# Kernel optimization log

Hardware: AMD Instinct MI355X
Metric: run time of the kernel (lower is better)

Reference implementation:

```python
import jax, jax.numpy as jnp
import numpy as np

QMAX = 7.0            # int4 narrow range: [-7, 7]
SCALING_MIN_VAL = 2e-16


def fake_quant_weight_per_channel(w):
    """Brevitas CommonIntWeightPerChannelQuant, bit_width=4.

    Per-output-channel float scale from abs-max stats, narrow-range signed
    int4 round+clamp, then dequantize. STE so gradients pass through.
    w: [O, I, KH, KW]
    """
    amax = jnp.max(jnp.abs(w), axis=(1, 2, 3), keepdims=True)   # [O,1,1,1]
    scale = jnp.maximum(amax / QMAX, SCALING_MIN_VAL)
    wq = jnp.clip(jnp.round(w / scale), -QMAX, QMAX) * scale
    # straight-through estimator (matches Brevitas round_ste backward)
    return w + jax.lax.stop_gradient(wq - w)


def setup_inputs() -> dict:
    key = jax.random.key(0)
    kx, kw = jax.random.split(key)
    x = jax.random.normal(kx, (32, 256, 56, 56), dtype=jnp.float32)
    # conv weight [out_channels, in_channels, kh, kw]
    w = jax.random.normal(kw, (256, 256, 3, 3), dtype=jnp.float32) * 0.05
    return {"x": x, "w": w}


def reference(x, w):
    wq = fake_quant_weight_per_channel(w)
    return jax.lax.conv_general_dilated(
        x, wq,
        window_strides=(1, 1),
        padding=((1, 1), (1, 1)),
        dimension_numbers=("NCHW", "OIHW", "NCHW"),
    )
```

## Files before the change

kernel.cpp:

```cpp
#include <hip/hip_runtime.h>
#include <cstdint>
#include <cstddef>

typedef __bf16 bf16x8 __attribute__((ext_vector_type(8)));
typedef float  f32x4  __attribute__((ext_vector_type(4)));
typedef int    i32x4  __attribute__((ext_vector_type(4)));

#define QMAX 7.0f
#define SCALE_MIN 2e-16f

__global__ __launch_bounds__(256) void quant_w_kernel(const float* __restrict__ w,
                                                      __bf16* __restrict__ wq) {
    const int o = blockIdx.x;
    const int t = threadIdx.x;
    const float* wo = w + (size_t)o * 2304;

    float vals[9];
    float m = 0.f;
    #pragma unroll
    for (int i = 0; i < 9; ++i) {
        float v = wo[t + i * 256];
        vals[i] = v;
        m = fmaxf(m, fabsf(v));
    }
    #pragma unroll
    for (int off = 32; off >= 1; off >>= 1) m = fmaxf(m, __shfl_down(m, off));
    __shared__ float red[4];
    __shared__ float s_scale;
    if ((t & 63) == 0) red[t >> 6] = m;
    __syncthreads();
    if (t == 0) {
        float am = fmaxf(fmaxf(red[0], red[1]), fmaxf(red[2], red[3]));
        s_scale = fmaxf(am / QMAX, SCALE_MIN);
    }
    __syncthreads();
    const float scale = s_scale;

    #pragma unroll
    for (int i = 0; i < 9; ++i) {
        int idx = t + i * 256;
        int c = idx / 9;
        int tap = idx - c * 9;
        float q = rintf(vals[i] / scale);
        q = fminf(QMAX, fmaxf(-QMAX, q));
        wq[(size_t)tap * 65536 + (size_t)o * 256 + c] = (__bf16)(q * scale);
    }
}

__global__ __launch_bounds__(256) void convert_x_kernel(const float* __restrict__ x,
                                                        __bf16* __restrict__ xpad) {
    __shared__ float tile[32][33];
    const int n  = blockIdx.z;
    const int c0 = blockIdx.y * 32;
    const int p0 = blockIdx.x * 32;
    const int tx = threadIdx.x & 31;
    const int ty = threadIdx.x >> 5;

    #pragma unroll
    for (int r = 0; r < 4; ++r) {
        int c = c0 + ty + r * 8;
        tile[ty + r * 8][tx] = x[((size_t)(n * 256 + c)) * 3136 + p0 + tx];
    }
    __syncthreads();
    #pragma unroll
    for (int r = 0; r < 4; ++r) {
        int p = p0 + ty + r * 8;
        int h = p / 56, wcol = p - h * 56;
        xpad[(((size_t)n * 58 + h + 1) * 58 + (wcol + 1)) * 256 + c0 + tx] =
            (__bf16)tile[tx][ty + r * 8];
    }
}

__global__ __launch_bounds__(256) void zero_halo_kernel(__bf16* __restrict__ xpad) {
    const int t = blockIdx.x * 256 + threadIdx.x;
    const int cvec = t & 31;
    const int r    = t >> 5;
    const int n    = r / 228;
    const int pos  = r - n * 228;
    if (n >= 32) return;
    int h, wcol;
    if      (pos < 58)  { h = 0;          wcol = pos; }
    else if (pos < 116) { h = 57;         wcol = pos - 58; }
    else if (pos < 172) { h = pos - 115;  wcol = 0; }
    else                { h = pos - 171;  wcol = 57; }
    i32x4* dst = (i32x4*)(xpad + (((size_t)n * 58 + h) * 58 + wcol) * 256);
    dst[cvec] = (i32x4){0, 0, 0, 0};
}

__device__ __forceinline__ void gload_lds16(const void* g, void* l) {
    __builtin_amdgcn_global_load_lds((const __attribute__((address_space(1))) void*)g,
                                     (__attribute__((address_space(3))) void*)l,
                                     16, 0, 0);
}

__global__ __launch_bounds__(256) void conv_mfma_kernel(const __bf16* __restrict__ xpad,
                                                        const __bf16* __restrict__ wq,
                                                        float* __restrict__ out) {
    __shared__ __align__(16) char Ash[128 * 128];
    __shared__ __align__(16) char Bsh[128 * 128];

    const int tid  = threadIdx.x;
    const int wv   = tid >> 6;
    const int lane = tid & 63;
    const int bp   = blockIdx.x;
    const int n    = bp / 25;
    const int p0   = (bp - n * 25) * 128;
    const int o0   = blockIdx.y * 128;

    const int srow   = wv * 8 + (lane >> 3);
    const int schunk = (lane & 7) ^ (lane >> 3);
    const int selem  = schunk * 8;

    const __bf16* pA = wq + (size_t)(o0 + srow) * 256 + selem;
    const __bf16* pB[4];
    #pragma unroll
    for (int j = 0; j < 4; ++j) {
        int p = p0 + srow + j * 32;
        if (p > 3135) p = 3135;
        int h = p / 56, wcol = p - h * 56;
        pB[j] = xpad + (((size_t)n * 58 + h) * 58 + wcol) * 256 + selem;
    }

    const int wr = wv >> 1;
    const int wc = wv & 1;

    const int a_rowbyte = (wr * 64 + (lane & 15)) * 128;
    const int b_rowbyte = (wc * 64 + (lane & 15)) * 128;
    int kx[2];
    #pragma unroll
    for (int s = 0; s < 2; ++s)
        kx[s] = ((s * 4 + (lane >> 4)) ^ (lane & 7)) * 16;

    f32x4 acc[4][4];
    #pragma unroll
    for (int m = 0; m < 4; ++m)
        #pragma unroll
        for (int nf = 0; nf < 4; ++nf)
            acc[m][nf] = (f32x4){0.f, 0.f, 0.f, 0.f};

    for (int tap = 0; tap < 9; ++tap) {
        const int kh = tap / 3, kw = tap - kh * 3;
        const size_t aoff0 = (size_t)tap * 65536;
        const size_t boff0 = (size_t)(kh * 58 + kw) * 256;
        #pragma unroll
        for (int cc = 0; cc < 4; ++cc) {
            const size_t aoff = aoff0 + cc * 64;
            const size_t boff = boff0 + cc * 64;
            #pragma unroll
            for (int j = 0; j < 4; ++j) {
                gload_lds16(pB[j] + boff, Bsh + (wv * 8 + j * 32) * 128);
                gload_lds16(pA + j * 8192 + aoff, Ash + (wv * 8 + j * 32) * 128);
            }
            __syncthreads();

            #pragma unroll
            for (int s = 0; s < 2; ++s) {
                bf16x8 a[4], b[4];
                #pragma unroll
                for (int m = 0; m < 4; ++m)
                    a[m] = *(const bf16x8*)(Ash + a_rowbyte + m * 2048 + kx[s]);
                #pragma unroll
                for (int nf = 0; nf < 4; ++nf)
                    b[nf] = *(const bf16x8*)(Bsh + b_rowbyte + nf * 2048 + kx[s]);
                #pragma unroll
                for (int m = 0; m < 4; ++m)
                    #pragma unroll
                    for (int nf = 0; nf < 4; ++nf)
                        acc[m][nf] = __builtin_amdgcn_mfma_f32_16x16x32_bf16(
                            a[m], b[nf], acc[m][nf], 0, 0, 0);
            }
            __syncthreads();
        }
    }

    #pragma unroll
    for (int m = 0; m < 4; ++m) {
        const int obase = o0 + wr * 64 + m * 16 + (lane >> 4) * 4;
        #pragma unroll
        for (int nf = 0; nf < 4; ++nf) {
            const int p = p0 + wc * 64 + nf * 16 + (lane & 15);
            if (p < 3136) {
                #pragma unroll
                for (int r = 0; r < 4; ++r)
                    out[((size_t)(n * 256 + obase + r)) * 3136 + p] = acc[m][nf][r];
            }
        }
    }
}

__global__ __launch_bounds__(256) void conv_naive_kernel(const float* __restrict__ x,
                                                         const float* __restrict__ w,
                                                         float* __restrict__ out) {
    const int n = blockIdx.z;
    const int o = blockIdx.y;
    const int strip = blockIdx.x;
    __shared__ float wqs[2304];
    __shared__ float red[4];
    __shared__ float s_scale;
    const float* wo = w + (size_t)o * 2304;
    float m = 0.f;
    for (int i = threadIdx.x; i < 2304; i += 256) m = fmaxf(m, fabsf(wo[i]));
    #pragma unroll
    for (int off = 32; off >= 1; off >>= 1) m = fmaxf(m, __shfl_down(m, off));
    if ((threadIdx.x & 63) == 0) red[threadIdx.x >> 6] = m;
    __syncthreads();
    if (threadIdx.x == 0) {
        float am = fmaxf(fmaxf(red[0], red[1]), fmaxf(red[2], red[3]));
        s_scale = fmaxf(am / QMAX, SCALE_MIN);
    }
    __syncthreads();
    const float scale = s_scale;
    for (int i = threadIdx.x; i < 2304; i += 256) {
        float q = rintf(wo[i] / scale);
        q = fminf(QMAX, fmaxf(-QMAX, q));
        wqs[i] = q * scale;
    }
    __syncthreads();
    int p = strip * 256 + threadIdx.x;
    if (p >= 3136) return;
    int h = p / 56, wcol = p - h * 56;
    float acc = 0.f;
    for (int c = 0; c < 256; ++c) {
        const float* xc = x + ((size_t)(n * 256 + c)) * 3136;
        const float* wk = wqs + c * 9;
        #pragma unroll
        for (int kh = 0; kh < 3; ++kh) {
            int hh = h + kh - 1;
            if (hh < 0 || hh > 55) continue;
            #pragma unroll
            for (int kw = 0; kw < 3; ++kw) {
                int ww2 = wcol + kw - 1;
                if (ww2 < 0 || ww2 > 55) continue;
                acc += xc[hh * 56 + ww2] * wk[kh * 3 + kw];
            }
        }
    }
    out[((size_t)(n * 256 + o)) * 3136 + p] = acc;
}

extern "C" void kernel_launch(void* const* d_in, const int* in_sizes, int n_in,
                              void* d_out, int out_size, void* d_ws, size_t ws_size,
                              hipStream_t stream) {
    const float* x = (const float*)d_in[0];
    const float* w = (const float*)d_in[1];
    float* out = (float*)d_out;

    const size_t WQ_BYTES   = 9ull * 256 * 256 * 2;
    const size_t XPAD_OFF   = WQ_BYTES;
    const size_t XPAD_BYTES = 32ull * 58 * 58 * 256 * 2;

    if (ws_size >= XPAD_OFF + XPAD_BYTES) {
        __bf16* wq   = (__bf16*)d_ws;
        __bf16* xpad = (__bf16*)((char*)d_ws + XPAD_OFF);
        zero_halo_kernel<<<912, 256, 0, stream>>>(xpad);
        quant_w_kernel<<<256, 256, 0, stream>>>(w, wq);
        convert_x_kernel<<<dim3(98, 8, 32), 256, 0, stream>>>(x, xpad);
        conv_mfma_kernel<<<dim3(800, 2), 256, 0, stream>>>(xpad, wq, out);
    } else {
        conv_naive_kernel<<<dim3(13, 256, 32), 256, 0, stream>>>(x, w, out);
    }
}
```

Measured before the change: 191.8 us.

## Rewrite conv GEMM as 256x256 double-buffered tile with 32x32 MFMA

```diff
diff --git a/kernel.cpp b/kernel.cpp
--- a/kernel.cpp
+++ b/kernel.cpp
@@ -4,10 +4,14 @@
 
 typedef __bf16 bf16x8 __attribute__((ext_vector_type(8)));
 typedef float  f32x4  __attribute__((ext_vector_type(4)));
+typedef float  f32x16 __attribute__((ext_vector_type(16)));
 typedef int    i32x4  __attribute__((ext_vector_type(4)));
 
 #define QMAX 7.0f
 #define SCALE_MIN 2e-16f
+
+#define BAR()    asm volatile("s_barrier" ::: "memory")
+#define WAITV0() asm volatile("s_waitcnt vmcnt(0)" ::: "memory")
 
 __global__ __launch_bounds__(256) void quant_w_kernel(const float* __restrict__ w,
                                                       __bf16* __restrict__ wq) {
@@ -93,96 +97,165 @@
                                      16, 0, 0);
 }
 
-__global__ __launch_bounds__(256) void conv_mfma_kernel(const __bf16* __restrict__ xpad,
-                                                        const __bf16* __restrict__ wq,
-                                                        float* __restrict__ out) {
-    __shared__ __align__(16) char Ash[128 * 128];
-    __shared__ __align__(16) char Bsh[128 * 128];
-
+__global__ __launch_bounds__(512, 2) void conv_mfma_kernel(const __bf16* __restrict__ xpad,
+                                                           const __bf16* __restrict__ wq,
+                                                           float* __restrict__ out) {
+    extern __shared__ __align__(16) char lds[];
     const int tid  = threadIdx.x;
     const int wv   = tid >> 6;
     const int lane = tid & 63;
-    const int bp   = blockIdx.x;
-    const int n    = bp / 25;
-    const int p0   = (bp - n * 25) * 128;
-    const int o0   = blockIdx.y * 128;
-
-    const int srow   = wv * 8 + (lane >> 3);
+    const int bid  = blockIdx.x;
+    const int swz  = (bid & 7) * 49 + (bid >> 3);
+    const int p0   = swz * 256;
+
+    const int wr = wv >> 2;
+    const int wc = wv & 3;
+
+    const int srow  = wv * 8 + (lane >> 3);
     const int schunk = (lane & 7) ^ (lane >> 3);
-    const int selem  = schunk * 8;
-
-    const __bf16* pA = wq + (size_t)(o0 + srow) * 256 + selem;
+    const __bf16* pAg = wq + (size_t)srow * 256 + schunk * 8;
     const __bf16* pB[4];
     #pragma unroll
-    for (int j = 0; j < 4; ++j) {
-        int p = p0 + srow + j * 32;
-        if (p > 3135) p = 3135;
-        int h = p / 56, wcol = p - h * 56;
-        pB[j] = xpad + (((size_t)n * 58 + h) * 58 + wcol) * 256 + selem;
-    }
-
-    const int wr = wv >> 1;
-    const int wc = wv & 1;
-
-    const int a_rowbyte = (wr * 64 + (lane & 15)) * 128;
-    const int b_rowbyte = (wc * 64 + (lane & 15)) * 128;
-    int kx[2];
-    #pragma unroll
-    for (int s = 0; s < 2; ++s)
-        kx[s] = ((s * 4 + (lane >> 4)) ^ (lane & 7)) * 16;
-
-    f32x4 acc[4][4];
+    for (int p = 0; p < 4; ++p) {
+        int pos = p0 + p * 64 + srow;
+        int ni = pos / 3136;
+        int hw = pos - ni * 3136;
+        int h = hw / 56, w = hw - h * 56;
+        pB[p] = xpad + (((size_t)ni * 58 + h) * 58 + w) * 256 + schunk * 8;
+    }
+
+    const int hi = lane >> 5;
+    int kxo[4];
+    #pragma unroll
+    for (int ks = 0; ks < 4; ++ks)
+        kxo[ks] = ((ks * 2 + hi) ^ (lane & 7)) * 16;
+    const int arowb = (wr * 128 + (lane & 31)) * 128;
+    const int browb = (wc * 64  + (lane & 31)) * 128;
+
+    f32x16 acc[4][2];
     #pragma unroll
     for (int m = 0; m < 4; ++m)
         #pragma unroll
-        for (int nf = 0; nf < 4; ++nf)
-            acc[m][nf] = (f32x4){0.f, 0.f, 0.f, 0.f};
-
-    for (int tap = 0; tap < 9; ++tap) {
-        const int kh = tap / 3, kw = tap - kh * 3;
-        const size_t aoff0 = (size_t)tap * 65536;
-        const size_t boff0 = (size_t)(kh * 58 + kw) * 256;
-        #pragma unroll
-        for (int cc = 0; cc < 4; ++cc) {
-            const size_t aoff = aoff0 + cc * 64;
-            const size_t boff = boff0 + cc * 64;
+        for (int n = 0; n < 2; ++n)
+            acc[m][n] = (f32x16)(0.f);
+
+    {
+        char* wa = lds;
+        char* wb = lds + 32768;
+        #pragma unroll
+        for (int p = 0; p < 4; ++p) {
+            gload_lds16(pAg + p * 16384, wa + (p * 64 + wv * 8) * 128);
+            gload_lds16(pB[p],           wb + (p * 64 + wv * 8) * 128);
+        }
+        WAITV0();
+        BAR();
+    }
+
+    for (int s = 0; s < 36; ++s) {
+        const int cur = s & 1;
+        const char* Ard = lds + (cur ? 65536 : 0);
+        const char* Brd = Ard + 32768;
+        char* Awr = lds + (cur ? 0 : 65536);
+        char* Bwr = Awr + 32768;
+        const bool stg = (s < 35);
+        int aoffN = 0, boffN = 0;
+        if (stg) {
+            const int sn = s + 1;
+            const int tapN = sn >> 2, ccN = sn & 3;
+            const int khN = tapN / 3, kwN = tapN - khN * 3;
+            aoffN = tapN * 65536 + ccN * 64;
+            boffN = (khN * 58 + kwN) * 256 + ccN * 64;
+        }
+
+        bf16x8 a0[4], a1[4], b0[4], b1[4];
+
+        if (stg) {
+            gload_lds16(pAg + 0 * 16384 + aoffN, Awr + (0 * 64 + wv * 8) * 128);
+            gload_lds16(pB[0] + boffN,           Bwr + (0 * 64 + wv * 8) * 128);
+        }
+        #pragma unroll
+        for (int ks = 0; ks < 4; ++ks) {
+            a0[ks] = *(const bf16x8*)(Ard + arowb + 0 * 4096 + kxo[ks]);
+            a1[ks] = *(const bf16x8*)(Ard + arowb + 1 * 4096 + kxo[ks]);
+            b0[ks] = *(const bf16x8*)(Brd + browb + 0 * 4096 + kxo[ks]);
+        }
+        BAR();
+        __builtin_amdgcn_s_setprio(1);
+        #pragma unroll
+        for (int ks = 0; ks < 4; ++ks) {
+            acc[0][0] = __builtin_amdgcn_mfma_f32_32x32x16_bf16(a0[ks], b0[ks], acc[0][0], 0, 0, 0);
+            acc[1][0] = __builtin_amdgcn_mfma_f32_32x32x16_bf16(a1[ks], b0[ks], acc[1][0], 0, 0, 0);
+        }
+        __builtin_amdgcn_s_setprio(0);
+        BAR();
+
+        if (stg) {
+            gload_lds16(pAg + 1 * 16384 + aoffN, Awr + (1 * 64 + wv * 8) * 128);
+            gload_lds16(pB[1] + boffN,           Bwr + (1 * 64 + wv * 8) * 128);
+        }
+        #pragma unroll
+        for (int ks = 0; ks < 4; ++ks)
+            b1[ks] = *(const bf16x8*)(Brd + browb + 1 * 4096 + kxo[ks]);
+        BAR();
+        __builtin_amdgcn_s_setprio(1);
+        #pragma unroll
+        for (int ks = 0; ks < 4; ++ks) {
+            acc[0][1] = __builtin_amdgcn_mfma_f32_32x32x16_bf16(a0[ks], b1[ks], acc[0][1], 0, 0, 0);
+            acc[1][1] = __builtin_amdgcn_mfma_f32_32x32x16_bf16(a1[ks], b1[ks], acc[1][1], 0, 0, 0);
+        }
+        __builtin_amdgcn_s_setprio(0);
+        BAR();
+
+        if (stg) {
+            gload_lds16(pAg + 2 * 16384 + aoffN, Awr + (2 * 64 + wv * 8) * 128);
+            gload_lds16(pB[2] + boffN,           Bwr + (2 * 64 + wv * 8) * 128);
+        }
+        #pragma unroll
+        for (int ks = 0; ks < 4; ++ks) {
+            a0[ks] = *(const bf16x8*)(Ard + arowb + 2 * 4096 + kxo[ks]);
+            a1[ks] = *(const bf16x8*)(Ard + arowb + 3 * 4096 + kxo[ks]);
+        }
+        BAR();
+        __builtin_amdgcn_s_setprio(1);
+        #pragma unroll
+        for (int ks = 0; ks < 4; ++ks) {
+            acc[2][0] = __builtin_amdgcn_mfma_f32_32x32x16_bf16(a0[ks], b0[ks], acc[2][0], 0, 0, 0);
+            acc[3][0] = __builtin_amdgcn_mfma_f32_32x32x16_bf16(a1[ks], b0[ks], acc[3][0], 0, 0, 0);
+        }
+        __builtin_amdgcn_s_setprio(0);
+        BAR();
+
+        if (stg) {
+            gload_lds16(pAg + 3 * 16384 + aoffN, Awr + (3 * 64 + wv * 8) * 128);
+            gload_lds16(pB[3] + boffN,           Bwr + (3 * 64 + wv * 8) * 128);
+        }
+        BAR();
+        __builtin_amdgcn_s_setprio(1);
+        #pragma unroll
+        for (int ks = 0; ks < 4; ++ks) {
+            acc[2][1] = __builtin_amdgcn_mfma_f32_32x32x16_bf16(a0[ks], b1[ks], acc[2][1], 0, 0, 0);
+            acc[3][1] = __builtin_amdgcn_mfma_f32_32x32x16_bf16(a1[ks], b1[ks], acc[3][1], 0, 0, 0);
+        }
+        __builtin_amdgcn_s_setprio(0);
+        BAR();
+
+        WAITV0();
+        BAR();
+    }
+
+    #pragma unroll
+    for (int n = 0; n < 2; ++n) {
+        const int pos = p0 + wc * 64 + n * 32 + (lane & 31);
+        const int ni = pos / 3136;
+        const int hw = pos - ni * 3136;
+        float* ob = out + (size_t)ni * 802816 + hw;
+        #pragma unroll
+        for (int m = 0; m < 4; ++m) {
+            const int om = wr * 128 + m * 32 + 4 * hi;
             #pragma unroll
-            for (int j = 0; j < 4; ++j) {
-                gload_lds16(pB[j] + boff, Bsh + (wv * 8 + j * 32) * 128);
-                gload_lds16(pA + j * 8192 + aoff, Ash + (wv * 8 + j * 32) * 128);
-            }
-            __syncthreads();
-
-            #pragma unroll
-            for (int s = 0; s < 2; ++s) {
-                bf16x8 a[4], b[4];
-                #pragma unroll
-                for (int m = 0; m < 4; ++m)
-                    a[m] = *(const bf16x8*)(Ash + a_rowbyte + m * 2048 + kx[s]);
-                #pragma unroll
-                for (int nf = 0; nf < 4; ++nf)
-                    b[nf] = *(const bf16x8*)(Bsh + b_rowbyte + nf * 2048 + kx[s]);
-                #pragma unroll
-                for (int m = 0; m < 4; ++m)
-                    #pragma unroll
-                    for (int nf = 0; nf < 4; ++nf)
-                        acc[m][nf] = __builtin_amdgcn_mfma_f32_16x16x32_bf16(
-                            a[m], b[nf], acc[m][nf], 0, 0, 0);
-            }
-            __syncthreads();
-        }
-    }
-
-    #pragma unroll
-    for (int m = 0; m < 4; ++m) {
-        const int obase = o0 + wr * 64 + m * 16 + (lane >> 4) * 4;
-        #pragma unroll
-        for (int nf = 0; nf < 4; ++nf) {
-            const int p = p0 + wc * 64 + nf * 16 + (lane & 15);
-            if (p < 3136) {
-                #pragma unroll
-                for (int r = 0; r < 4; ++r)
-                    out[((size_t)(n * 256 + obase + r)) * 3136 + p] = acc[m][nf][r];
+            for (int r = 0; r < 16; ++r) {
+                const int o = om + (r & 3) + 8 * (r >> 2);
+                ob[(size_t)o * 3136] = acc[m][n][r];
             }
         }
     }
@@ -252,10 +325,12 @@
     if (ws_size >= XPAD_OFF + XPAD_BYTES) {
         __bf16* wq   = (__bf16*)d_ws;
         __bf16* xpad = (__bf16*)((char*)d_ws + XPAD_OFF);
+        hipFuncSetAttribute((const void*)conv_mfma_kernel,
+                            hipFuncAttributeMaxDynamicSharedMemorySize, 131072);
         zero_halo_kernel<<<912, 256, 0, stream>>>(xpad);
         quant_w_kernel<<<256, 256, 0, stream>>>(w, wq);
         convert_x_kernel<<<dim3(98, 8, 32), 256, 0, stream>>>(x, xpad);
-        conv_mfma_kernel<<<dim3(800, 2), 256, 0, stream>>>(xpad, wq, out);
+        conv_mfma_kernel<<<392, 512, 131072, stream>>>(xpad, wq, out);
     } else {
         conv_naive_kernel<<<dim3(13, 256, 32), 256, 0, stream>>>(x, w, out);
     }
```

After: 185.5 us. 3.3% less time.

## Restructure conv GEMM with 256x128 tiles and triple-buffered async LDS pipeline

Applied to the files above, without the earlier changes.

```diff
diff --git a/kernel.cpp b/kernel.cpp
--- a/kernel.cpp
+++ b/kernel.cpp
@@ -8,6 +8,9 @@
 
 #define QMAX 7.0f
 #define SCALE_MIN 2e-16f
+
+#define BAR()     asm volatile("s_barrier" ::: "memory")
+#define WAITVM(N) asm volatile("s_waitcnt vmcnt(" #N ")" ::: "memory")
 
 __global__ __launch_bounds__(256) void quant_w_kernel(const float* __restrict__ w,
                                                       __bf16* __restrict__ wq) {
@@ -93,97 +96,119 @@
                                      16, 0, 0);
 }
 
-__global__ __launch_bounds__(256) void conv_mfma_kernel(const __bf16* __restrict__ xpad,
-                                                        const __bf16* __restrict__ wq,
-                                                        float* __restrict__ out) {
-    __shared__ __align__(16) char Ash[128 * 128];
-    __shared__ __align__(16) char Bsh[128 * 128];
-
+__global__ __launch_bounds__(256, 2) void conv_mfma_kernel(const __bf16* __restrict__ xpad,
+                                                           const __bf16* __restrict__ wq,
+                                                           float* __restrict__ out) {
+    extern __shared__ __align__(16) char lds[];
     const int tid  = threadIdx.x;
     const int wv   = tid >> 6;
     const int lane = tid & 63;
-    const int bp   = blockIdx.x;
-    const int n    = bp / 25;
-    const int p0   = (bp - n * 25) * 128;
-    const int o0   = blockIdx.y * 128;
-
-    const int srow   = wv * 8 + (lane >> 3);
-    const int schunk = (lane & 7) ^ (lane >> 3);
-    const int selem  = schunk * 8;
-
-    const __bf16* pA = wq + (size_t)(o0 + srow) * 256 + selem;
-    const __bf16* pB[4];
-    #pragma unroll
-    for (int j = 0; j < 4; ++j) {
-        int p = p0 + srow + j * 32;
-        if (p > 3135) p = 3135;
-        int h = p / 56, wcol = p - h * 56;
-        pB[j] = xpad + (((size_t)n * 58 + h) * 58 + wcol) * 256 + selem;
-    }
-
-    const int wr = wv >> 1;
-    const int wc = wv & 1;
-
-    const int a_rowbyte = (wr * 64 + (lane & 15)) * 128;
-    const int b_rowbyte = (wc * 64 + (lane & 15)) * 128;
-    int kx[2];
-    #pragma unroll
-    for (int s = 0; s < 2; ++s)
-        kx[s] = ((s * 4 + (lane >> 4)) ^ (lane & 7)) * 16;
-
-    f32x4 acc[4][4];
-    #pragma unroll
-    for (int m = 0; m < 4; ++m)
-        #pragma unroll
-        for (int nf = 0; nf < 4; ++nf)
-            acc[m][nf] = (f32x4){0.f, 0.f, 0.f, 0.f};
-
-    for (int tap = 0; tap < 9; ++tap) {
-        const int kh = tap / 3, kw = tap - kh * 3;
-        const size_t aoff0 = (size_t)tap * 65536;
-        const size_t boff0 = (size_t)(kh * 58 + kw) * 256;
-        #pragma unroll
-        for (int cc = 0; cc < 4; ++cc) {
-            const size_t aoff = aoff0 + cc * 64;
-            const size_t boff = boff0 + cc * 64;
-            #pragma unroll
-            for (int j = 0; j < 4; ++j) {
-                gload_lds16(pB[j] + boff, Bsh + (wv * 8 + j * 32) * 128);
-                gload_lds16(pA + j * 8192 + aoff, Ash + (wv * 8 + j * 32) * 128);
-            }
-            __syncthreads();
-
-            #pragma unroll
-            for (int s = 0; s < 2; ++s) {
-                bf16x8 a[4], b[4];
-                #pragma unroll
-                for (int m = 0; m < 4; ++m)
-                    a[m] = *(const bf16x8*)(Ash + a_rowbyte + m * 2048 + kx[s]);
-                #pragma unroll
-                for (int nf = 0; nf < 4; ++nf)
-                    b[nf] = *(const bf16x8*)(Bsh + b_rowbyte + nf * 2048 + kx[s]);
-                #pragma unroll
-                for (int m = 0; m < 4; ++m)
-                    #pragma unroll
-                    for (int nf = 0; nf < 4; ++nf)
-                        acc[m][nf] = __builtin_amdgcn_mfma_f32_16x16x32_bf16(
-                            a[m], b[nf], acc[m][nf], 0, 0, 0);
-            }
-            __syncthreads();
-        }
-    }
-
-    #pragma unroll
-    for (int m = 0; m < 4; ++m) {
-        const int obase = o0 + wr * 64 + m * 16 + (lane >> 4) * 4;
-        #pragma unroll
-        for (int nf = 0; nf < 4; ++nf) {
-            const int p = p0 + wc * 64 + nf * 16 + (lane & 15);
-            if (p < 3136) {
-                #pragma unroll
-                for (int r = 0; r < 4; ++r)
-                    out[((size_t)(n * 256 + obase + r)) * 3136 + p] = acc[m][nf][r];
-            }
+    const int bid  = blockIdx.x;
+    const int swz  = (bid & 7) * 98 + (bid >> 3);
+    const int p0   = swz * 128;
+
+    const int wm = wv >> 1;
+    const int wn = wv & 1;
+
+    const int trow   = tid >> 2;
+    const int schunk = (tid & 3) ^ ((tid >> 5) & 3);
+    const __bf16* pA[4];
+    #pragma unroll
+    for (int j = 0; j < 4; ++j)
+        pA[j] = wq + (size_t)(j * 64 + trow) * 256 + schunk * 8;
+    const __bf16* pBs[2];
+    #pragma unroll
+    for (int j = 0; j < 2; ++j) {
+        int pos = p0 + j * 64 + trow;
+        int ni = pos / 3136;
+        int hw = pos - ni * 3136;
+        int h = hw / 56, w = hw - h * 56;
+        pBs[j] = xpad + (((size_t)ni * 58 + h) * 58 + w) * 256 + schunk * 8;
+    }
+    const int adst = wv * 1024;
+    const int bdst = 16384 + wv * 1024;
+
+    const int l15 = lane & 15;
+    const int aoff0 = l15 * 64 + (((lane >> 4) ^ ((lane >> 3) & 1)) << 4);
+    const int abase = wm * 8192;
+    const int bbase = 16384 + wn * 4096;
+
+    f32x4 acc[8][4];
+    #pragma unroll
+    for (int m = 0; m < 8; ++m)
+        #pragma unroll
+        for (int n = 0; n < 4; ++n)
+            acc[m][n] = (f32x4){0.f, 0.f, 0.f, 0.f};
+
+    #define STAGE(STEP, BUF)                                                  \
+        {                                                                     \
+            const int tap_ = (STEP) >> 3, cc_ = (STEP) & 7;                   \
+            const int kh_ = tap_ / 3, kw_ = tap_ - kh_ * 3;                   \
+            const size_t aoff_ = (size_t)tap_ * 65536 + cc_ * 32;             \
+            const size_t boff_ = (size_t)(kh_ * 58 + kw_) * 256 + cc_ * 32;   \
+            gload_lds16(pA[0] + aoff_, (BUF) + adst);                         \
+            gload_lds16(pA[1] + aoff_, (BUF) + adst + 4096);                  \
+            gload_lds16(pA[2] + aoff_, (BUF) + adst + 8192);                  \
+            gload_lds16(pA[3] + aoff_, (BUF) + adst + 12288);                 \
+            gload_lds16(pBs[0] + boff_, (BUF) + bdst);                        \
+            gload_lds16(pBs[1] + boff_, (BUF) + bdst + 4096);                 \
+        }
+
+    STAGE(0, lds);
+
+    int co = 0;
+    #pragma unroll 1
+    for (int s = 0; s < 72; ++s) {
+        int no = co + 24576; if (no == 73728) no = 0;
+        if (s < 71) {
+            STAGE(s + 1, lds + no);
+            WAITVM(6);
+        } else {
+            WAITVM(0);
+        }
+        BAR();
+        const char* B = lds + co;
+
+        bf16x8 a[4], b[4];
+        #pragma unroll
+        for (int m = 0; m < 4; ++m)
+            a[m] = *(const bf16x8*)(B + abase + m * 1024 + (aoff0 ^ ((m & 1) << 5)));
+        #pragma unroll
+        for (int n = 0; n < 4; ++n)
+            b[n] = *(const bf16x8*)(B + bbase + n * 1024 + (aoff0 ^ ((n & 1) << 5)));
+        __builtin_amdgcn_s_setprio(1);
+        #pragma unroll
+        for (int m = 0; m < 4; ++m)
+            #pragma unroll
+            for (int n = 0; n < 4; ++n)
+                acc[m][n] = __builtin_amdgcn_mfma_f32_16x16x32_bf16(a[m], b[n], acc[m][n], 0, 0, 0);
+        __builtin_amdgcn_s_setprio(0);
+        #pragma unroll
+        for (int m = 0; m < 4; ++m)
+            a[m] = *(const bf16x8*)(B + abase + (m + 4) * 1024 + (aoff0 ^ ((m & 1) << 5)));
+        __builtin_amdgcn_s_setprio(1);
+        #pragma unroll
+        for (int m = 0; m < 4; ++m)
+            #pragma unroll
+            for (int n = 0; n < 4; ++n)
+                acc[m + 4][n] = __builtin_amdgcn_mfma_f32_16x16x32_bf16(a[m], b[n], acc[m + 4][n], 0, 0, 0);
+        __builtin_amdgcn_s_setprio(0);
+        co = no;
+    }
+    #undef STAGE
+
+    #pragma unroll
+    for (int n = 0; n < 4; ++n) {
+        const int pos = p0 + wn * 64 + n * 16 + l15;
+        const int ni = pos / 3136;
+        const int hw = pos - ni * 3136;
+        float* ob = out + (size_t)ni * 802816 + hw;
+        #pragma unroll
+        for (int m = 0; m < 8; ++m) {
+            const int om = wm * 128 + m * 16 + (lane >> 4) * 4;
+            #pragma unroll
+            for (int r = 0; r < 4; ++r)
+                ob[(size_t)(om + r) * 3136] = acc[m][n][r];
         }
     }
 }
@@ -252,10 +277,12 @@
     if (ws_size >= XPAD_OFF + XPAD_BYTES) {
         __bf16* wq   = (__bf16*)d_ws;
         __bf16* xpad = (__bf16*)((char*)d_ws + XPAD_OFF);
+        hipFuncSetAttribute((const void*)conv_mfma_kernel,
+                            hipFuncAttributeMaxDynamicSharedMemorySize, 73728);
         zero_halo_kernel<<<912, 256, 0, stream>>>(xpad);
         quant_w_kernel<<<256, 256, 0, stream>>>(w, wq);
         convert_x_kernel<<<dim3(98, 8, 32), 256, 0, stream>>>(x, xpad);
-        conv_mfma_kernel<<<dim3(800, 2), 256, 0, stream>>>(xpad, wq, out);
+        conv_mfma_kernel<<<784, 256, 73728, stream>>>(xpad, wq, out);
     } else {
         conv_naive_kernel<<<dim3(13, 256, 32), 256, 0, stream>>>(x, w, out);
     }
```

After: 167.8 us. 1.14x faster.
